# Kernel tuning notes

Hardware: AMD Instinct MI355X
Metric: run time of the kernel (lower is better)

Reference implementation:

```python
import jax, jax.numpy as jnp
import numpy as np

NDIM = 4096      # ndim constructor arg; also hidden_node
BATCH = 2048
HID_F = 5        # hidden_feature (hardcoded in source)
STRIDE = 5       # encode_stride (hardcoded in source)


def _build_edges(ndim):
    # Faithful reproduction of the encoder edge construction in __init__.
    edges = []
    for j in range(ndim):
        c = j % ndim
        for i in range(c - STRIDE, c + STRIDE):
            edges.append([i % ndim, j])
    e = np.asarray(edges, dtype=np.int32).T  # [2, E], row=src, col=dst
    return e[0], e[1]


def setup_inputs() -> dict:
    key = jax.random.key(0)
    k1, k2, k3, k4, k5 = jax.random.split(key, 5)
    src, dst = _build_edges(NDIM)
    return {
        "x": jax.random.normal(k1, (BATCH, NDIM), jnp.float32),
        # PyG GraphConv((1, HID_F), HID_F): lin_rel Linear(1->HID_F, bias=True),
        # lin_root Linear(HID_F->HID_F, bias=False)
        "W_rel": jax.random.normal(k2, (HID_F, 1), jnp.float32) * 0.5,
        "b_rel": jax.random.normal(k3, (HID_F,), jnp.float32) * 0.1,
        "W_root": jax.random.normal(k4, (HID_F, HID_F), jnp.float32) * 0.1,
        # final Linear(ndim*HID_F -> ndim, bias=False)
        "W_final": jax.random.normal(k5, (NDIM, NDIM * HID_F), jnp.float32) * 0.01,
        "edge_src": jnp.asarray(src),
        "edge_dst": jnp.asarray(dst),
    }


def reference(x, W_rel, b_rel, W_root, W_final, edge_src, edge_dst):
    B, N = x.shape
    # gather source node features along edges: [B, E]
    vals = x[:, edge_src]
    # scatter-add into target nodes (sum aggregation): [B, N]
    agg = jax.ops.segment_sum(vals.T, edge_dst, num_segments=N).T
    # lin_rel (1 -> HID_F) applied to aggregated scalar feature
    z = agg[..., None] * W_rel[:, 0] + b_rel  # [B, N, HID_F]
    # lin_root applied to dst features z0 (zeros in this model) -- kept for faithfulness
    z0 = jnp.zeros((B, N, HID_F), x.dtype)
    z = z + z0 @ W_root.T
    z = jax.nn.relu(z)
    # final projection
    y = z.reshape(B, N * HID_F) @ W_final.T  # [B, N]
    return y
```

## Files before the change

### kernel.cpp

```cpp
#include <hip/hip_runtime.h>
#include <hip/hip_bf16.h>
#include <stdint.h>
#include <stddef.h>

#define NDIM  4096
#define BATCH 2048
#define HIDF  5
#define KDIM  (NDIM * HIDF)

typedef __bf16 bf16_t;
typedef __bf16 bf16x8 __attribute__((ext_vector_type(8)));
typedef float  f32x4  __attribute__((ext_vector_type(4)));

__device__ __forceinline__ void async_load_16B(const void* g, void* l) {
    __builtin_amdgcn_global_load_lds(
        (const __attribute__((address_space(1))) void*)g,
        (__attribute__((address_space(3))) void*)l,
        16, 0, 0);
}

__global__ void build_z(const float* __restrict__ x,
                        const float* __restrict__ W_rel,
                        const float* __restrict__ b_rel,
                        bf16_t* __restrict__ z)
{
    int idx = blockIdx.x * blockDim.x + threadIdx.x;
    int b = idx >> 12;
    int n = idx & (NDIM - 1);
    const float* xr = x + (size_t)b * NDIM;
    float agg = 0.f;
#pragma unroll
    for (int d = -5; d < 5; ++d)
        agg += xr[(n + d) & (NDIM - 1)];
    bf16_t* zr = z + (size_t)b * KDIM + n * HIDF;
#pragma unroll
    for (int f = 0; f < HIDF; ++f) {
        float v = fmaf(agg, W_rel[f], b_rel[f]);
        v = v > 0.f ? v : 0.f;
        zr[f] = (bf16_t)v;
    }
}

__global__ void cvt_w(const float* __restrict__ W, bf16_t* __restrict__ Wb,
                      int total8)
{
    int i = blockIdx.x * blockDim.x + threadIdx.x;
    int stride = gridDim.x * blockDim.x;
    for (; i < total8; i += stride) {
        const float* s = W + (size_t)i * 8;
        f32x4 v0 = *(const f32x4*)(s);
        f32x4 v1 = *(const f32x4*)(s + 4);
        bf16x8 pk;
        pk[0] = (bf16_t)v0[0]; pk[1] = (bf16_t)v0[1];
        pk[2] = (bf16_t)v0[2]; pk[3] = (bf16_t)v0[3];
        pk[4] = (bf16_t)v1[0]; pk[5] = (bf16_t)v1[1];
        pk[6] = (bf16_t)v1[2]; pk[7] = (bf16_t)v1[3];
        *(bf16x8*)(Wb + (size_t)i * 8) = pk;
    }
}

#define NT 160

__device__ __forceinline__ void stage_tile(const bf16_t* gA, const bf16_t* gB,
                                           char* As, char* Bs, int wid)
{
#pragma unroll
    for (int li = 0; li < 4; ++li) {
        async_load_16B(gA + (size_t)li * 64 * KDIM, As + li * 8192 + wid * 1024);
        async_load_16B(gB + (size_t)li * 64 * KDIM, Bs + li * 8192 + wid * 1024);
    }
}

__global__ __launch_bounds__(512, 2) void gemm8p(
    const bf16_t* __restrict__ Z,
    const bf16_t* __restrict__ Wb,
    float* __restrict__ Y,
    float* __restrict__ P)
{
    __shared__ char smem[131072];

    const int tid  = threadIdx.x;
    const int lane = tid & 63;
    const int wid  = tid >> 6;
    const int wr   = wid >> 2;
    const int wc   = wid & 3;

    const int bid   = blockIdx.x;
    const int split = bid & 1;
    const int tile  = bid >> 1;
    const int tm    = tile & 7;
    const int tn    = tile >> 3;
    const int m0    = tm * 256;
    const int n0    = tn * 256;
    const int kbase = split * (NT * 64);

    const int sr  = lane >> 3;
    const int scb = (lane & 7) ^ sr;
    const bf16_t* gA = Z  + (size_t)(m0 + wid * 8 + sr) * KDIM + kbase + scb * 8;
    const bf16_t* gB = Wb + (size_t)(n0 + wid * 8 + sr) * KDIM + kbase + scb * 8;

    const int r15  = lane & 15;
    const int xk   = (lane >> 4) << 4;
    const int xs   = (lane & 7) << 4;
    const int col0 = xk ^ xs;
    const int dcol = 64 - 2 * (col0 & 64);

    float* const out = split ? P : Y;

    f32x4 acc[8][4];
#pragma unroll
    for (int i = 0; i < 8; ++i)
#pragma unroll
        for (int j = 0; j < 4; ++j)
            acc[i][j] = (f32x4)0.f;

    stage_tile(gA,      gB,      smem,         smem + 32768, wid);
    stage_tile(gA + 64, gB + 64, smem + 65536, smem + 98304, wid);

    for (int u = 0; u < NT; ++u) {
        if (u >= 1 && u + 1 < NT) {
            const int nk = (u + 1) * 64;
            char* ab = smem + (((u + 1) & 1) ? 65536 : 0);
            stage_tile(gA + nk, gB + nk, ab, ab + 32768, wid);
        }
        if (u + 1 < NT) asm volatile("s_waitcnt vmcnt(8)" ::: "memory");
        else            asm volatile("s_waitcnt vmcnt(0)" ::: "memory");
        __builtin_amdgcn_s_barrier();

        const char* Ab = smem + ((u & 1) ? 65536 : 0);
        const char* pA = Ab + (wr * 128 + r15) * 128 + col0;
        const char* pB = Ab + 32768 + (wc * 64 + r15) * 128 + col0;

        bf16x8 a[4][2], b[4][2];

#pragma unroll
        for (int mi = 0; mi < 4; ++mi) {
            a[mi][0] = *(const bf16x8*)(pA + mi * 2048);
            a[mi][1] = *(const bf16x8*)(pA + mi * 2048 + dcol);
        }
#pragma unroll
        for (int ni = 0; ni < 2; ++ni) {
            b[ni][0] = *(const bf16x8*)(pB + ni * 2048);
            b[ni][1] = *(const bf16x8*)(pB + ni * 2048 + dcol);
        }
        __builtin_amdgcn_s_barrier();
        __builtin_amdgcn_s_setprio(1);
#pragma unroll
        for (int mi = 0; mi < 4; ++mi)
#pragma unroll
            for (int ni = 0; ni < 2; ++ni)
#pragma unroll
                for (int s = 0; s < 2; ++s)
                    acc[mi][ni] = __builtin_amdgcn_mfma_f32_16x16x32_bf16(
                        a[mi][s], b[ni][s], acc[mi][ni], 0, 0, 0);
        __builtin_amdgcn_s_setprio(0);

#pragma unroll
        for (int ni = 2; ni < 4; ++ni) {
            b[ni][0] = *(const bf16x8*)(pB + ni * 2048);
            b[ni][1] = *(const bf16x8*)(pB + ni * 2048 + dcol);
        }
        __builtin_amdgcn_s_barrier();
        __builtin_amdgcn_s_setprio(1);
#pragma unroll
        for (int mi = 0; mi < 4; ++mi)
#pragma unroll
            for (int ni = 2; ni < 4; ++ni)
#pragma unroll
                for (int s = 0; s < 2; ++s)
                    acc[mi][ni] = __builtin_amdgcn_mfma_f32_16x16x32_bf16(
                        a[mi][s], b[ni][s], acc[mi][ni], 0, 0, 0);
        __builtin_amdgcn_s_setprio(0);

#pragma unroll
        for (int mi = 0; mi < 4; ++mi) {
            a[mi][0] = *(const bf16x8*)(pA + (mi + 4) * 2048);
            a[mi][1] = *(const bf16x8*)(pA + (mi + 4) * 2048 + dcol);
        }
        __builtin_amdgcn_s_barrier();
        __builtin_amdgcn_s_setprio(1);
#pragma unroll
        for (int mi = 0; mi < 4; ++mi)
#pragma unroll
            for (int ni = 0; ni < 2; ++ni)
#pragma unroll
                for (int s = 0; s < 2; ++s)
                    acc[mi + 4][ni] = __builtin_amdgcn_mfma_f32_16x16x32_bf16(
                        a[mi][s], b[ni][s], acc[mi + 4][ni], 0, 0, 0);
        __builtin_amdgcn_s_setprio(0);

        __builtin_amdgcn_s_barrier();
        __builtin_amdgcn_s_setprio(1);
#pragma unroll
        for (int mi = 0; mi < 4; ++mi)
#pragma unroll
            for (int ni = 2; ni < 4; ++ni)
#pragma unroll
                for (int s = 0; s < 2; ++s)
                    acc[mi + 4][ni] = __builtin_amdgcn_mfma_f32_16x16x32_bf16(
                        a[mi][s], b[ni][s], acc[mi + 4][ni], 0, 0, 0);
        __builtin_amdgcn_s_setprio(0);

        __builtin_amdgcn_s_barrier();
    }

    const int crow = m0 + wr * 128 + (lane >> 4) * 4;
    const int ccol = n0 + wc * 64 + (lane & 15);
#pragma unroll
    for (int mi = 0; mi < 8; ++mi)
#pragma unroll
        for (int ni = 0; ni < 4; ++ni) {
            float* cp = out + (size_t)(crow + mi * 16) * NDIM + ccol + ni * 16;
#pragma unroll
            for (int rr = 0; rr < 4; ++rr)
                cp[(size_t)rr * NDIM] = acc[mi][ni][rr];
        }
}

__global__ void add_y(float* __restrict__ y, const float* __restrict__ p, int n4)
{
    int i = blockIdx.x * blockDim.x + threadIdx.x;
    int st = gridDim.x * blockDim.x;
    for (; i < n4; i += st) {
        f32x4 a = ((const f32x4*)y)[i];
        f32x4 b = ((const f32x4*)p)[i];
        ((f32x4*)y)[i] = a + b;
    }
}

#define BM 128
#define BN 128
#define BK 64

__global__ __launch_bounds__(256) void gemm_bb(
    const bf16_t* __restrict__ Z,
    const bf16_t* __restrict__ Wb,
    float*        __restrict__ Y)
{
    __shared__ bf16_t As[BM * BK];
    __shared__ bf16_t Bs[BN * BK];

    const int tid  = threadIdx.x;
    const int lane = tid & 63;
    const int wid  = tid >> 6;
    const int bidm = blockIdx.x & 15;
    const int bidn = blockIdx.x >> 4;
    const int bm0 = bidm * BM;
    const int bn0 = bidn * BN;
    const int wr = wid >> 1, wc = wid & 1;

    f32x4 acc[4][4];
#pragma unroll
    for (int i = 0; i < 4; ++i)
#pragma unroll
        for (int j = 0; j < 4; ++j)
            acc[i][j] = (f32x4)0.f;

    const int arow_l = lane >> 3;
    const int acol_l = (lane & 7) * 8;

    for (int kt = 0; kt < KDIM / BK; ++kt) {
        const int k0 = kt * BK;
#pragma unroll
        for (int r = 0; r < 4; ++r) {
            const int chunk = wid * 4 + r;
            const int row   = chunk * 8 + arow_l;
            async_load_16B(Z + (size_t)(bm0 + row) * KDIM + k0 + acol_l,
                           (void*)(As + chunk * 512));
            async_load_16B(Wb + (size_t)(bn0 + row) * KDIM + k0 + acol_l,
                           (void*)(Bs + chunk * 512));
        }
        __syncthreads();
#pragma unroll
        for (int s = 0; s < 2; ++s) {
            bf16x8 af[4], bfr[4];
            const int ko = s * 32 + (lane >> 4) * 8;
#pragma unroll
            for (int mi = 0; mi < 4; ++mi)
                af[mi] = *(const bf16x8*)(As + (wr * 64 + mi * 16 + (lane & 15)) * BK + ko);
#pragma unroll
            for (int ni = 0; ni < 4; ++ni)
                bfr[ni] = *(const bf16x8*)(Bs + (wc * 64 + ni * 16 + (lane & 15)) * BK + ko);
#pragma unroll
            for (int mi = 0; mi < 4; ++mi)
#pragma unroll
                for (int ni = 0; ni < 4; ++ni)
                    acc[mi][ni] = __builtin_amdgcn_mfma_f32_16x16x32_bf16(
                        af[mi], bfr[ni], acc[mi][ni], 0, 0, 0);
        }
        __syncthreads();
    }

    const int crow = bm0 + wr * 64 + (lane >> 4) * 4;
    const int ccol = bn0 + wc * 64 + (lane & 15);
#pragma unroll
    for (int mi = 0; mi < 4; ++mi)
#pragma unroll
        for (int ni = 0; ni < 4; ++ni) {
            float* cp = Y + (size_t)(crow + mi * 16) * NDIM + ccol + ni * 16;
#pragma unroll
            for (int r = 0; r < 4; ++r)
                cp[(size_t)r * NDIM] = acc[mi][ni][r];
        }
}

__global__ __launch_bounds__(256) void gemm_zw(
    const bf16_t* __restrict__ Z,
    const float*  __restrict__ W,
    float*        __restrict__ Y)
{
    __shared__ bf16_t As[BM * BK];
    __shared__ bf16_t Bs[BN * BK];

    const int tid  = threadIdx.x;
    const int lane = tid & 63;
    const int wid  = tid >> 6;
    const int bidm = blockIdx.x & 15;
    const int bidn = blockIdx.x >> 4;
    const int bm0 = bidm * BM;
    const int bn0 = bidn * BN;
    const int wr = wid >> 1, wc = wid & 1;

    f32x4 acc[4][4];
#pragma unroll
    for (int i = 0; i < 4; ++i)
#pragma unroll
        for (int j = 0; j < 4; ++j)
            acc[i][j] = (f32x4)0.f;

    const int arow_l = lane >> 3;
    const int acol_l = (lane & 7) * 8;

    for (int kt = 0; kt < KDIM / BK; ++kt) {
        const int k0 = kt * BK;
#pragma unroll
        for (int r = 0; r < 4; ++r) {
            const int chunk = wid * 4 + r;
            const int row   = chunk * 8 + arow_l;
            async_load_16B(Z + (size_t)(bm0 + row) * KDIM + k0 + acol_l,
                           (void*)(As + chunk * 512));
        }
#pragma unroll
        for (int r = 0; r < 4; ++r) {
            const int chunk = wid * 4 + r;
            const int row   = chunk * 8 + arow_l;
            const float* src = W + (size_t)(bn0 + row) * KDIM + k0 + acol_l;
            f32x4 v0 = *(const f32x4*)(src);
            f32x4 v1 = *(const f32x4*)(src + 4);
            bf16x8 pk;
            pk[0] = (bf16_t)v0[0]; pk[1] = (bf16_t)v0[1];
            pk[2] = (bf16_t)v0[2]; pk[3] = (bf16_t)v0[3];
            pk[4] = (bf16_t)v1[0]; pk[5] = (bf16_t)v1[1];
            pk[6] = (bf16_t)v1[2]; pk[7] = (bf16_t)v1[3];
            *(bf16x8*)(Bs + chunk * 512 + lane * 8) = pk;
        }
        __syncthreads();
#pragma unroll
        for (int s = 0; s < 2; ++s) {
            bf16x8 af[4], bfr[4];
            const int ko = s * 32 + (lane >> 4) * 8;
#pragma unroll
            for (int mi = 0; mi < 4; ++mi)
                af[mi] = *(const bf16x8*)(As + (wr * 64 + mi * 16 + (lane & 15)) * BK + ko);
#pragma unroll
            for (int ni = 0; ni < 4; ++ni)
                bfr[ni] = *(const bf16x8*)(Bs + (wc * 64 + ni * 16 + (lane & 15)) * BK + ko);
#pragma unroll
            for (int mi = 0; mi < 4; ++mi)
#pragma unroll
                for (int ni = 0; ni < 4; ++ni)
                    acc[mi][ni] = __builtin_amdgcn_mfma_f32_16x16x32_bf16(
                        af[mi], bfr[ni], acc[mi][ni], 0, 0, 0);
        }
        __syncthreads();
    }

    const int crow = bm0 + wr * 64 + (lane >> 4) * 4;
    const int ccol = bn0 + wc * 64 + (lane & 15);
#pragma unroll
    for (int mi = 0; mi < 4; ++mi)
#pragma unroll
        for (int ni = 0; ni < 4; ++ni) {
            float* cp = Y + (size_t)(crow + mi * 16) * NDIM + ccol + ni * 16;
#pragma unroll
            for (int r = 0; r < 4; ++r)
                cp[(size_t)r * NDIM] = acc[mi][ni][r];
        }
}

extern "C" void kernel_launch(void* const* d_in, const int* in_sizes, int n_in,
                              void* d_out, int out_size, void* d_ws, size_t ws_size,
                              hipStream_t stream)
{
    const float* x      = (const float*)d_in[0];
    const float* W_rel  = (const float*)d_in[1];
    const float* b_rel  = (const float*)d_in[2];
    const float* W_fin  = (const float*)d_in[4];

    const size_t z_bytes  = (size_t)BATCH * KDIM * sizeof(bf16_t);
    const size_t wb_bytes = (size_t)NDIM  * KDIM * sizeof(bf16_t);
    const size_t p_bytes  = (size_t)BATCH * NDIM * sizeof(float);

    char* ws = (char*)d_ws;
    bf16_t* z  = (bf16_t*)ws;
    float*  y  = (float*)d_out;

    build_z<<<(BATCH * NDIM) / 256, 256, 0, stream>>>(x, W_rel, b_rel, z);

    if (ws_size >= z_bytes + wb_bytes + p_bytes) {
        bf16_t* Wb = (bf16_t*)(ws + z_bytes);
        float*  P  = (float*)(ws + z_bytes + wb_bytes);
        cvt_w<<<2048, 256, 0, stream>>>(W_fin, Wb, (int)((size_t)NDIM * KDIM / 8));
        gemm8p<<<256, 512, 0, stream>>>(z, Wb, y, P);
        add_y<<<2048, 256, 0, stream>>>(y, P, (BATCH * NDIM) / 4);
    } else if (ws_size >= z_bytes + wb_bytes) {
        bf16_t* Wb = (bf16_t*)(ws + z_bytes);
        cvt_w<<<2048, 256, 0, stream>>>(W_fin, Wb, (int)((size_t)NDIM * KDIM / 8));
        gemm_bb<<<(NDIM / BN) * (BATCH / BM), 256, 0, stream>>>(z, Wb, y);
    } else {
        gemm_zw<<<(NDIM / BN) * (BATCH / BM), 256, 0, stream>>>(z, W_fin, y);
    }
}
```

Measured before the change: 469.5 us.

## Interleave next-tile async loads across MFMA phases with one-ahead prefetch

```diff
diff --git a/kernel.cpp b/kernel.cpp
--- a/kernel.cpp
+++ b/kernel.cpp
@@ -61,16 +61,6 @@
 
 #define NT 160
 
-__device__ __forceinline__ void stage_tile(const bf16_t* gA, const bf16_t* gB,
-                                           char* As, char* Bs, int wid)
-{
-#pragma unroll
-    for (int li = 0; li < 4; ++li) {
-        async_load_16B(gA + (size_t)li * 64 * KDIM, As + li * 8192 + wid * 1024);
-        async_load_16B(gB + (size_t)li * 64 * KDIM, Bs + li * 8192 + wid * 1024);
-    }
-}
-
 __global__ __launch_bounds__(512, 2) void gemm8p(
     const bf16_t* __restrict__ Z,
     const bf16_t* __restrict__ Wb,
@@ -114,24 +104,30 @@
         for (int j = 0; j < 4; ++j)
             acc[i][j] = (f32x4)0.f;
 
-    stage_tile(gA,      gB,      smem,         smem + 32768, wid);
-    stage_tile(gA + 64, gB + 64, smem + 65536, smem + 98304, wid);
-
-    for (int u = 0; u < NT; ++u) {
-        if (u >= 1 && u + 1 < NT) {
-            const int nk = (u + 1) * 64;
-            char* ab = smem + (((u + 1) & 1) ? 65536 : 0);
-            stage_tile(gA + nk, gB + nk, ab, ab + 32768, wid);
-        }
-        if (u + 1 < NT) asm volatile("s_waitcnt vmcnt(8)" ::: "memory");
-        else            asm volatile("s_waitcnt vmcnt(0)" ::: "memory");
-        __builtin_amdgcn_s_barrier();
-
-        const char* Ab = smem + ((u & 1) ? 65536 : 0);
-        const char* pA = Ab + (wr * 128 + r15) * 128 + col0;
-        const char* pB = Ab + 32768 + (wc * 64 + r15) * 128 + col0;
+#pragma unroll
+    for (int li = 0; li < 4; ++li) {
+        async_load_16B(gA + (size_t)li * 64 * KDIM, smem + li * 8192 + wid * 1024);
+        async_load_16B(gB + (size_t)li * 64 * KDIM, smem + 32768 + li * 8192 + wid * 1024);
+    }
+
+    for (int g = 0; g < NT; ++g) {
+        char* const cb = smem + ((g & 1) ? 65536 : 0);
+        char* const nb = smem + ((g & 1) ? 0 : 65536);
+        const char* const pA = cb + (wr * 128 + r15) * 128 + col0;
+        const char* const pB = cb + 32768 + (wc * 64 + r15) * 128 + col0;
+        const bf16_t* const nA = gA + (size_t)(g + 1) * 64;
+        const bf16_t* const nB = gB + (size_t)(g + 1) * 64;
 
         bf16x8 a[4][2], b[4][2];
+
+        if (g + 1 < NT) {
+            async_load_16B(nA, nb + wid * 1024);
+            async_load_16B(nB, nb + 32768 + wid * 1024);
+            asm volatile("s_waitcnt vmcnt(2)" ::: "memory");
+        } else {
+            asm volatile("s_waitcnt vmcnt(0)" ::: "memory");
+        }
+        __builtin_amdgcn_s_barrier();
 
 #pragma unroll
         for (int mi = 0; mi < 4; ++mi) {
@@ -144,6 +140,8 @@
             b[ni][1] = *(const bf16x8*)(pB + ni * 2048 + dcol);
         }
         __builtin_amdgcn_s_barrier();
+        asm volatile("s_waitcnt lgkmcnt(0)" ::: "memory");
+        __builtin_amdgcn_sched_barrier(0);
         __builtin_amdgcn_s_setprio(1);
 #pragma unroll
         for (int mi = 0; mi < 4; ++mi)
@@ -154,13 +152,20 @@
                     acc[mi][ni] = __builtin_amdgcn_mfma_f32_16x16x32_bf16(
                         a[mi][s], b[ni][s], acc[mi][ni], 0, 0, 0);
         __builtin_amdgcn_s_setprio(0);
+        __builtin_amdgcn_s_barrier();
 
 #pragma unroll
         for (int ni = 2; ni < 4; ++ni) {
             b[ni][0] = *(const bf16x8*)(pB + ni * 2048);
             b[ni][1] = *(const bf16x8*)(pB + ni * 2048 + dcol);
         }
-        __builtin_amdgcn_s_barrier();
+        if (g + 1 < NT) {
+            async_load_16B(nA + (size_t)64 * KDIM, nb + 8192 + wid * 1024);
+            async_load_16B(nB + (size_t)64 * KDIM, nb + 32768 + 8192 + wid * 1024);
+        }
+        __builtin_amdgcn_s_barrier();
+        asm volatile("s_waitcnt lgkmcnt(0)" ::: "memory");
+        __builtin_amdgcn_sched_barrier(0);
         __builtin_amdgcn_s_setprio(1);
 #pragma unroll
         for (int mi = 0; mi < 4; ++mi)
@@ -171,13 +176,20 @@
                     acc[mi][ni] = __builtin_amdgcn_mfma_f32_16x16x32_bf16(
                         a[mi][s], b[ni][s], acc[mi][ni], 0, 0, 0);
         __builtin_amdgcn_s_setprio(0);
+        __builtin_amdgcn_s_barrier();
 
 #pragma unroll
         for (int mi = 0; mi < 4; ++mi) {
             a[mi][0] = *(const bf16x8*)(pA + (mi + 4) * 2048);
             a[mi][1] = *(const bf16x8*)(pA + (mi + 4) * 2048 + dcol);
         }
-        __builtin_amdgcn_s_barrier();
+        if (g + 1 < NT) {
+            async_load_16B(nA + (size_t)128 * KDIM, nb + 16384 + wid * 1024);
+            async_load_16B(nB + (size_t)128 * KDIM, nb + 32768 + 16384 + wid * 1024);
+        }
+        __builtin_amdgcn_s_barrier();
+        asm volatile("s_waitcnt lgkmcnt(0)" ::: "memory");
+        __builtin_amdgcn_sched_barrier(0);
         __builtin_amdgcn_s_setprio(1);
 #pragma unroll
         for (int mi = 0; mi < 4; ++mi)
@@ -188,7 +200,12 @@
                     acc[mi + 4][ni] = __builtin_amdgcn_mfma_f32_16x16x32_bf16(
                         a[mi][s], b[ni][s], acc[mi + 4][ni], 0, 0, 0);
         __builtin_amdgcn_s_setprio(0);
-
+        __builtin_amdgcn_s_barrier();
+
+        if (g + 1 < NT) {
+            async_load_16B(nA + (size_t)192 * KDIM, nb + 24576 + wid * 1024);
+            async_load_16B(nB + (size_t)192 * KDIM, nb + 32768 + 24576 + wid * 1024);
+        }
         __builtin_amdgcn_s_barrier();
         __builtin_amdgcn_s_setprio(1);
 #pragma unroll
@@ -200,7 +217,6 @@
                     acc[mi + 4][ni] = __builtin_amdgcn_mfma_f32_16x16x32_bf16(
                         a[mi][s], b[ni][s], acc[mi + 4][ni], 0, 0, 0);
         __builtin_amdgcn_s_setprio(0);
-
         __builtin_amdgcn_s_barrier();
     }
 
```

After: 447.8 us. 1.05x faster.
